# Performance work log

Hardware: AMD Instinct MI355X
Metric: run time of the kernel (lower is better)

## Reference

```python
import jax, jax.numpy as jnp
import numpy as np

N_NODES = 100000
N_EDGES = 1600000
IN_C, HID_C, OUT_C = 128, 128, 64


def setup_inputs() -> dict:
    key = jax.random.key(0)
    k1, k2, k3, k4 = jax.random.split(key, 4)
    x = jax.random.normal(k1, (N_NODES, IN_C), dtype=jnp.float32)
    edge_index = jax.random.randint(k2, (2, N_EDGES), 0, N_NODES, dtype=jnp.int32)
    # Glorot-style init scale for the linear weights (matches PyG GCNConv default)
    W1 = jax.random.normal(k3, (IN_C, HID_C), dtype=jnp.float32) * (1.0 / np.sqrt(IN_C))
    b1 = jnp.zeros((HID_C,), dtype=jnp.float32)
    W2 = jax.random.normal(k4, (HID_C, OUT_C), dtype=jnp.float32) * (1.0 / np.sqrt(HID_C))
    b2 = jnp.zeros((OUT_C,), dtype=jnp.float32)
    return {"x": x, "edge_index": edge_index, "W1": W1, "b1": b1, "W2": W2, "b2": b2}


def _gcn_norm(edge_index, num_nodes):
    """Add self-loops and compute symmetric normalization deg^-1/2[src]*deg^-1/2[dst]."""
    src, dst = edge_index[0], edge_index[1]
    loop = jnp.arange(num_nodes, dtype=src.dtype)
    src_f = jnp.concatenate([src, loop])
    dst_f = jnp.concatenate([dst, loop])
    ones = jnp.ones_like(dst_f, dtype=jnp.float32)
    deg = jax.ops.segment_sum(ones, dst_f, num_segments=num_nodes)  # in-degree incl. self-loop
    deg_inv_sqrt = jnp.where(deg > 0, jax.lax.rsqrt(deg), 0.0)
    norm = deg_inv_sqrt[src_f] * deg_inv_sqrt[dst_f]  # [E+N]
    return src_f, dst_f, norm


def _gcn_conv(x, W, b, src_f, dst_f, norm, num_nodes):
    h = x @ W                              # [N, C_out] linear transform first
    msg = h[src_f] * norm[:, None]         # gather + scale, [E+N, C_out]
    agg = jax.ops.segment_sum(msg, dst_f, num_segments=num_nodes)  # scatter-add
    return agg + b


def reference(x, edge_index, W1, b1, W2, b2):
    n = x.shape[0]
    src_f, dst_f, norm = _gcn_norm(edge_index, n)
    h = jax.nn.relu(_gcn_conv(x, W1, b1, src_f, dst_f, norm, n))
    out = _gcn_conv(h, W2, b2, src_f, dst_f, norm, n)
    return out
```

## Files before the change

kernel.cpp:

```cpp
#include <hip/hip_runtime.h>


constexpr int BLK = 256;
constexpr int PCAP = 2560;
constexpr int CPAD = 16;
constexpr int CHUNK = 6144;
constexpr int NBMAX = 800;


__global__ __launch_bounds__(256)
void bucket_sort_kernel(const int* __restrict__ src, const int* __restrict__ dst,
                        int* __restrict__ bcnt, unsigned* __restrict__ ebuf,
                        int e, int nbuck) {
    __shared__ unsigned stage[CHUNK];
    __shared__ unsigned short keys[CHUNK];
    __shared__ int hist[NBMAX];
    __shared__ int excl[NBMAX];
    __shared__ int gbase[NBMAX];
    __shared__ int wsum[256];

    const int t = threadIdx.x;
    const int base = blockIdx.x * CHUNK;
    const int cnt = min(CHUNK, e - base);

    for (int i = t; i < nbuck; i += 256) hist[i] = 0;
    __syncthreads();

    for (int i = t; i < cnt; i += 256) atomicAdd(&hist[dst[base + i] >> 7], 1);
    __syncthreads();

    const int b0 = t * 4;
    int s0 = 0, s1 = 0, s2 = 0, s3 = 0;
    if (b0 < nbuck)     s0 = hist[b0];
    if (b0 + 1 < nbuck) s1 = hist[b0 + 1];
    if (b0 + 2 < nbuck) s2 = hist[b0 + 2];
    if (b0 + 3 < nbuck) s3 = hist[b0 + 3];
    wsum[t] = s0 + s1 + s2 + s3;
    __syncthreads();
    for (int off = 1; off < 256; off <<= 1) {
        int v = (t >= off) ? wsum[t - off] : 0;
        __syncthreads();
        wsum[t] += v;
        __syncthreads();
    }
    int run = (t > 0) ? wsum[t - 1] : 0;
    if (b0 < nbuck)     { excl[b0]     = run; hist[b0]     = run; run += s0; }
    if (b0 + 1 < nbuck) { excl[b0 + 1] = run; hist[b0 + 1] = run; run += s1; }
    if (b0 + 2 < nbuck) { excl[b0 + 2] = run; hist[b0 + 2] = run; run += s2; }
    if (b0 + 3 < nbuck) { excl[b0 + 3] = run; hist[b0 + 3] = run; run += s3; }
    __syncthreads();

    for (int i = t; i < cnt; i += 256) {
        int s = src[base + i], d = dst[base + i];
        int bb = d >> 7;
        int p = atomicAdd(&hist[bb], 1);
        stage[p] = ((unsigned)s << 7) | (unsigned)(d & 127);
        keys[p] = (unsigned short)bb;
    }
    __syncthreads();

    if (b0 < nbuck)     { int c = hist[b0]     - excl[b0];     gbase[b0]     = c ? atomicAdd(&bcnt[b0 * CPAD], c)       : 0; }
    if (b0 + 1 < nbuck) { int c = hist[b0 + 1] - excl[b0 + 1]; gbase[b0 + 1] = c ? atomicAdd(&bcnt[(b0 + 1) * CPAD], c) : 0; }
    if (b0 + 2 < nbuck) { int c = hist[b0 + 2] - excl[b0 + 2]; gbase[b0 + 2] = c ? atomicAdd(&bcnt[(b0 + 2) * CPAD], c) : 0; }
    if (b0 + 3 < nbuck) { int c = hist[b0 + 3] - excl[b0 + 3]; gbase[b0 + 3] = c ? atomicAdd(&bcnt[(b0 + 3) * CPAD], c) : 0; }
    __syncthreads();

    for (int i = t; i < cnt; i += 256) {
        int bb = keys[i];
        int p = gbase[bb] + (i - excl[bb]);
        if (p < PCAP) ebuf[(size_t)bb * PCAP + p] = stage[i];
    }
}


__global__ __launch_bounds__(256)
void build_kernel(const unsigned* __restrict__ ebuf, const int* __restrict__ bcnt,
                  float* __restrict__ dis, int2* __restrict__ rp,
                  int* __restrict__ esrc, int n) {
    __shared__ int packed[PCAP];
    __shared__ int stage[PCAP];
    __shared__ int hist[128];
    __shared__ int excl[128];
    __shared__ int cur[128];

    const int b = blockIdx.x, t = threadIdx.x;
    const int base = b << 7;
    const int nloc = min(128, n - base);
    const int tot = min(bcnt[b * CPAD], PCAP);

    if (t < 128) hist[t] = 0;
    __syncthreads();

    const unsigned* eb = ebuf + (size_t)b * PCAP;
    for (int i = t; i < tot; i += 256) {
        int v = (int)eb[i];
        packed[i] = v;
        atomicAdd(&hist[v & 127], 1);
    }
    __syncthreads();

    if (t < 128) excl[t] = hist[t];
    __syncthreads();
    for (int off = 1; off < 128; off <<= 1) {
        int v = (t >= off && t < 128) ? excl[t - off] : 0;
        __syncthreads();
        if (t < 128) excl[t] += v;
        __syncthreads();
    }

    if (t < 128) {
        int deg = hist[t];
        int start = excl[t] - deg;
        cur[t] = start;
        if (t < nloc) {
            dis[base + t] = rsqrtf((float)(deg + 1));
            int gs = b * PCAP + start;
            rp[base + t] = make_int2(gs, gs + deg);
        }
    }
    __syncthreads();

    for (int i = t; i < tot; i += 256) {
        int v = packed[i];
        int p = atomicAdd(&cur[v & 127], 1);
        stage[p] = v >> 7;
    }
    __syncthreads();

    for (int i = t; i < tot; i += 256) esrc[b * PCAP + i] = stage[i];
}


__device__ __forceinline__ unsigned short f2bf(float f) {
    unsigned u = __float_as_uint(f);
    u += 0x7fffu + ((u >> 16) & 1u);
    return (unsigned short)(u >> 16);
}
__device__ __forceinline__ float bflo(unsigned u) { return __uint_as_float(u << 16); }
__device__ __forceinline__ float bfhi(unsigned u) { return __uint_as_float(u & 0xffff0000u); }
__device__ __forceinline__ unsigned pk2(short a, short b) {
    return (unsigned)(unsigned short)a | ((unsigned)(unsigned short)b << 16);
}

__device__ __forceinline__ void split2(float v, short& hi, short& lo) {
    unsigned short h = f2bf(v);
    float hf = __uint_as_float(((unsigned)h) << 16);
    hi = (short)h;
    lo = (short)f2bf(v - hf);
}

typedef __attribute__((ext_vector_type(8))) short bf16x8;
typedef __attribute__((ext_vector_type(4))) float f32x4;
#define MFMA_B16(a, b, c) __builtin_amdgcn_mfma_f32_16x16x32_bf16(a, b, c, 0, 0, 0)

__device__ __forceinline__ void split8(const float4& a, const float4& b, bf16x8& h, bf16x8& l) {
    short hh, ll;
    split2(a.x, hh, ll); h[0] = hh; l[0] = ll;
    split2(a.y, hh, ll); h[1] = hh; l[1] = ll;
    split2(a.z, hh, ll); h[2] = hh; l[2] = ll;
    split2(a.w, hh, ll); h[3] = hh; l[3] = ll;
    split2(b.x, hh, ll); h[4] = hh; l[4] = ll;
    split2(b.y, hh, ll); h[5] = hh; l[5] = ll;
    split2(b.z, hh, ll); h[6] = hh; l[6] = ll;
    split2(b.w, hh, ll); h[7] = hh; l[7] = ll;
}


__global__ void prep_b_kernel(const float* __restrict__ W1, const float* __restrict__ W2,
                              unsigned short* __restrict__ B1h, unsigned short* __restrict__ B1l,
                              unsigned short* __restrict__ B2h, unsigned short* __restrict__ B2l) {
    const int c = blockIdx.x;
    const int k = threadIdx.x;
    short h, l;
    if (c < 128) {
        split2(W1[(size_t)k * 128 + c], h, l);
        B1h[c * 128 + k] = (unsigned short)h;
        B1l[c * 128 + k] = (unsigned short)l;
    } else {
        const int c2 = c - 128;
        split2(W2[(size_t)k * 64 + c2], h, l);
        B2h[c2 * 128 + k] = (unsigned short)h;
        B2l[c2 * 128 + k] = (unsigned short)l;
    }
}


constexpr int BAS = 72;

template <int COLS, bool PRESPLIT>
__global__ __launch_bounds__(256, 4)
void gemm_mfma(const float* __restrict__ Af, const unsigned short* __restrict__ Ah,
               const unsigned short* __restrict__ Al,
               const unsigned short* __restrict__ Bh, const unsigned short* __restrict__ Bl,
               const float* __restrict__ dis, unsigned* __restrict__ Cb, int nrows) {
    constexpr int CT = COLS / 16;
    constexpr int BE = COLS * BAS;
    constexpr int CSC = COLS + 8;
    constexpr int SMEM = (2 * BE * 2 > 128 * CSC * 2) ? 2 * BE * 2 : 128 * CSC * 2;

    __shared__ __align__(16) char smem[SMEM];
    short* sBh = (short*)smem;
    short* sBl = sBh + BE;

    const int t = threadIdx.x;
    const int rowbase = blockIdx.x * 128;
    const int wave = t >> 6;
    const int lane = t & 63;
    const int quad = lane >> 4;
    const int l16 = lane & 15;

    const int gr0 = rowbase + wave * 32 + l16;
    const int gr1 = gr0 + 16;

    f32x4 acc[2][CT];
#pragma unroll
    for (int rt = 0; rt < 2; ++rt)
#pragma unroll
        for (int ct = 0; ct < CT; ++ct) {
            f32x4 z = {0.f, 0.f, 0.f, 0.f};
            acc[rt][ct] = z;
        }

    for (int half = 0; half < 2; ++half) {
        {
            constexpr int NV = COLS * 8;
            uint4* dh = (uint4*)sBh;
            uint4* dl = (uint4*)sBl;
            const uint4* gh = (const uint4*)Bh;
            const uint4* gl = (const uint4*)Bl;
            for (int idx = t; idx < NV; idx += 256) {
                int c = idx >> 3, kq = idx & 7;
                int gidx = c * 16 + half * 8 + kq;
                int didx = c * 9 + kq;
                dh[didx] = gh[gidx];
                dl[didx] = gl[gidx];
            }
        }
        __syncthreads();

#pragma unroll
        for (int kc = 0; kc < 2; ++kc) {
            const int ko = kc * 32 + quad * 8;
            bf16x8 ah0, al0, ah1, al1;
            if constexpr (PRESPLIT) {
                bf16x8 z = {0, 0, 0, 0, 0, 0, 0, 0};
                ah0 = z; al0 = z; ah1 = z; al1 = z;
                if (gr0 < nrows) {
                    ah0 = *(const bf16x8*)&Ah[(size_t)gr0 * 128 + half * 64 + ko];
                    al0 = *(const bf16x8*)&Al[(size_t)gr0 * 128 + half * 64 + ko];
                }
                if (gr1 < nrows) {
                    ah1 = *(const bf16x8*)&Ah[(size_t)gr1 * 128 + half * 64 + ko];
                    al1 = *(const bf16x8*)&Al[(size_t)gr1 * 128 + half * 64 + ko];
                }
            } else {
                float4 va = {0.f, 0.f, 0.f, 0.f}, vb = va, vc = va, vd = va;
                if (gr0 < nrows) {
                    const float4* ap = (const float4*)(Af + (size_t)gr0 * 128 + half * 64 + ko);
                    va = ap[0]; vb = ap[1];
                }
                if (gr1 < nrows) {
                    const float4* ap = (const float4*)(Af + (size_t)gr1 * 128 + half * 64 + ko);
                    vc = ap[0]; vd = ap[1];
                }
                split8(va, vb, ah0, al0);
                split8(vc, vd, ah1, al1);
            }
#pragma unroll
            for (int ct = 0; ct < CT; ++ct) {
                const int bo = (ct * 16 + l16) * BAS + ko;
                bf16x8 bh = *(const bf16x8*)&sBh[bo];
                bf16x8 bl = *(const bf16x8*)&sBl[bo];
                acc[0][ct] = MFMA_B16(ah0, bh, acc[0][ct]);
                acc[1][ct] = MFMA_B16(ah1, bh, acc[1][ct]);
                acc[0][ct] = MFMA_B16(al0, bh, acc[0][ct]);
                acc[1][ct] = MFMA_B16(al1, bh, acc[1][ct]);
                acc[0][ct] = MFMA_B16(ah0, bl, acc[0][ct]);
                acc[1][ct] = MFMA_B16(ah1, bl, acc[1][ct]);
            }
        }
        __syncthreads();
    }

    short* Cs = (short*)smem;
    float sv[2][4];
#pragma unroll
    for (int rt = 0; rt < 2; ++rt)
#pragma unroll
        for (int r = 0; r < 4; ++r) {
            int rr = rowbase + wave * 32 + rt * 16 + quad * 4 + r;
            sv[rt][r] = (rr < nrows) ? dis[rr] : 0.f;
        }
#pragma unroll
    for (int rt = 0; rt < 2; ++rt)
#pragma unroll
        for (int ct = 0; ct < CT; ++ct) {
            const int rb = wave * 32 + rt * 16 + quad * 4;
            const int c = ct * 16 + l16;
#pragma unroll
            for (int r = 0; r < 4; ++r)
                Cs[(rb + r) * CSC + c] = (short)f2bf(sv[rt][r] * acc[rt][ct][r]);
        }
    __syncthreads();

    {
        const int row = t >> 1, hf = t & 1;
        const int gr = rowbase + row;
        if (gr < nrows) {
            const uint4* cr = (const uint4*)&Cs[row * CSC + hf * (COLS / 2)];
            uint4* dstp = (uint4*)Cb + (size_t)gr * (COLS / 8) + hf * (COLS / 16);
#pragma unroll
            for (int i = 0; i < COLS / 16; ++i) dstp[i] = cr[i];
        }
    }
}


template <int C, bool SPLITOUT>
__global__ __launch_bounds__(256)
void gather_add_kernel(const int2* __restrict__ rp, const int* __restrict__ esrc,
                       const float* __restrict__ dis, const unsigned* __restrict__ hs,
                       const float* __restrict__ bias, float* __restrict__ out,
                       unsigned short* __restrict__ outh, unsigned short* __restrict__ outl,
                       int n) {
    constexpr int L = C / 8;
    const int gid = blockIdx.x * BLK + threadIdx.x;
    const int node = gid / L;
    const int lane = gid % L;
    if (node >= n) return;

    const uint4* h4 = (const uint4*)hs;
    const int2 se = rp[node];

    float acc[8];
    {
        uint4 v = h4[(size_t)node * L + lane];
        acc[0] = bflo(v.x); acc[1] = bfhi(v.x);
        acc[2] = bflo(v.y); acc[3] = bfhi(v.y);
        acc[4] = bflo(v.z); acc[5] = bfhi(v.z);
        acc[6] = bflo(v.w); acc[7] = bfhi(v.w);
    }

#define ACC8(v)                                           \
    acc[0] += bflo(v.x); acc[1] += bfhi(v.x);             \
    acc[2] += bflo(v.y); acc[3] += bfhi(v.y);             \
    acc[4] += bflo(v.z); acc[5] += bfhi(v.z);             \
    acc[6] += bflo(v.w); acc[7] += bfhi(v.w);

    int k = se.x;
    const int end = se.y;
    for (; k + 3 < end; k += 4) {
        int s0 = esrc[k], s1 = esrc[k + 1], s2 = esrc[k + 2], s3 = esrc[k + 3];
        uint4 v0 = h4[(size_t)s0 * L + lane];
        uint4 v1 = h4[(size_t)s1 * L + lane];
        uint4 v2 = h4[(size_t)s2 * L + lane];
        uint4 v3 = h4[(size_t)s3 * L + lane];
        ACC8(v0) ACC8(v1) ACC8(v2) ACC8(v3)
    }
    for (; k < end; ++k) {
        uint4 v = h4[(size_t)esrc[k] * L + lane];
        ACC8(v)
    }
#undef ACC8

    const float di = dis[node];
    const float4 bj0 = ((const float4*)bias)[lane * 2 + 0];
    const float4 bj1 = ((const float4*)bias)[lane * 2 + 1];
    float v0 = fmaf(di, acc[0], bj0.x), v1 = fmaf(di, acc[1], bj0.y);
    float v2 = fmaf(di, acc[2], bj0.z), v3 = fmaf(di, acc[3], bj0.w);
    float v4 = fmaf(di, acc[4], bj1.x), v5 = fmaf(di, acc[5], bj1.y);
    float v6 = fmaf(di, acc[6], bj1.z), v7 = fmaf(di, acc[7], bj1.w);

    if constexpr (SPLITOUT) {
        short h0, l0, h1, l1, h2, l2, h3, l3, h4s, l4, h5, l5, h6, l6, h7, l7;
        split2(fmaxf(v0, 0.f), h0, l0); split2(fmaxf(v1, 0.f), h1, l1);
        split2(fmaxf(v2, 0.f), h2, l2); split2(fmaxf(v3, 0.f), h3, l3);
        split2(fmaxf(v4, 0.f), h4s, l4); split2(fmaxf(v5, 0.f), h5, l5);
        split2(fmaxf(v6, 0.f), h6, l6); split2(fmaxf(v7, 0.f), h7, l7);
        uint4 oh, ol;
        oh.x = pk2(h0, h1); oh.y = pk2(h2, h3); oh.z = pk2(h4s, h5); oh.w = pk2(h6, h7);
        ol.x = pk2(l0, l1); ol.y = pk2(l2, l3); ol.z = pk2(l4, l5);  ol.w = pk2(l6, l7);
        ((uint4*)outh)[(size_t)node * L + lane] = oh;
        ((uint4*)outl)[(size_t)node * L + lane] = ol;
    } else {
        float4 o0 = make_float4(v0, v1, v2, v3);
        float4 o1 = make_float4(v4, v5, v6, v7);
        float4* o4 = (float4*)out;
        o4[(size_t)node * (C / 4) + lane * 2 + 0] = o0;
        o4[(size_t)node * (C / 4) + lane * 2 + 1] = o1;
    }
}


extern "C" void kernel_launch(void* const* d_in, const int* in_sizes, int n_in,
                              void* d_out, int out_size, void* d_ws, size_t ws_size,
                              hipStream_t stream) {
    const float* x  = (const float*)d_in[0];
    const int*   ei = (const int*)d_in[1];
    const float* W1 = (const float*)d_in[2];
    const float* b1 = (const float*)d_in[3];
    const float* W2 = (const float*)d_in[4];
    const float* b2 = (const float*)d_in[5];
    float* out = (float*)d_out;

    const int n = in_sizes[0] / 128;
    const int e = in_sizes[1] / 2;
    const int* src = ei;
    const int* dst = ei + e;

    char* ws = (char*)d_ws;
    float*    dis  = (float*)   (ws + 0x0);
    int2*     rp   = (int2*)    (ws + 0x80000);
    int*      bcnt = (int*)     (ws + 0x180000);
    unsigned short* B1h = (unsigned short*)(ws + 0x1A0000);
    unsigned short* B1l = (unsigned short*)(ws + 0x1A8000);
    unsigned short* B2h = (unsigned short*)(ws + 0x1B0000);
    unsigned short* B2l = (unsigned short*)(ws + 0x1B4000);
    int*      esrc = (int*)     (ws + 0x280000);
    unsigned* hb   = (unsigned*)(ws + 0xB00000);
    unsigned short* A2h = (unsigned short*)(ws + 0x2400000);
    unsigned short* A2l = (unsigned short*)(ws + 0x3C80000);
    unsigned* ebuf = (unsigned*)(ws + 0x2400000);
    unsigned* h2b  = hb;

    const int nbuck = (n + 127) >> 7;
    const int nb_g = (n + 127) / 128;

    hipMemsetAsync(bcnt, 0, (size_t)nbuck * CPAD * 4, stream);
    prep_b_kernel<<<192, 128, 0, stream>>>(W1, W2, B1h, B1l, B2h, B2l);
    bucket_sort_kernel<<<(e + CHUNK - 1) / CHUNK, 256, 0, stream>>>(src, dst, bcnt, ebuf, e, nbuck);
    build_kernel<<<nbuck, 256, 0, stream>>>(ebuf, bcnt, dis, rp, esrc, n);

    gemm_mfma<128, false><<<nb_g, 256, 0, stream>>>(x, nullptr, nullptr, B1h, B1l, dis, hb, n);
    gather_add_kernel<128, true><<<(n * 16 + BLK - 1) / BLK, BLK, 0, stream>>>(
        rp, esrc, dis, hb, b1, nullptr, A2h, A2l, n);

    gemm_mfma<64, true><<<nb_g, 256, 0, stream>>>(nullptr, A2h, A2l, B2h, B2l, dis, h2b, n);
    gather_add_kernel<64, false><<<(n * 8 + BLK - 1) / BLK, BLK, 0, stream>>>(
        rp, esrc, dis, h2b, b2, out, nullptr, nullptr, n);
}
```

Measured before the change: 274.5 us.

## Fuse layer-1 aggregation with layer-2 GEMM and widen per-thread gather work

Layer-1 neighbor aggregation is fused with the layer-2 MFMA GEMM. Each block aggregates 32 nodes, writes the ReLU'd hi/lo bf16 split into LDS, and multiplies by W2 directly. This removes the global write and re-read of the split A2 activations and one kernel launch. Both gather kernels now give each thread 16 channels instead of 8, so fewer threads share a node, which changes memory-level parallelism and register pressure. In the fused kernel the B2 fragments are read straight from global memory rather than staged in LDS.

Measured after the change: 266.4 us. 3.0% less time.

```diff
diff --git a/kernel.cpp b/kernel.cpp
--- a/kernel.cpp
+++ b/kernel.cpp
@@ -187,12 +187,11 @@
 
 constexpr int BAS = 72;
 
-template <int COLS, bool PRESPLIT>
 __global__ __launch_bounds__(256, 4)
-void gemm_mfma(const float* __restrict__ Af, const unsigned short* __restrict__ Ah,
-               const unsigned short* __restrict__ Al,
+void gemm_mfma(const float* __restrict__ Af,
                const unsigned short* __restrict__ Bh, const unsigned short* __restrict__ Bl,
                const float* __restrict__ dis, unsigned* __restrict__ Cb, int nrows) {
+    constexpr int COLS = 128;
     constexpr int CT = COLS / 16;
     constexpr int BE = COLS * BAS;
     constexpr int CSC = COLS + 8;
@@ -242,30 +241,17 @@
         for (int kc = 0; kc < 2; ++kc) {
             const int ko = kc * 32 + quad * 8;
             bf16x8 ah0, al0, ah1, al1;
-            if constexpr (PRESPLIT) {
-                bf16x8 z = {0, 0, 0, 0, 0, 0, 0, 0};
-                ah0 = z; al0 = z; ah1 = z; al1 = z;
-                if (gr0 < nrows) {
-                    ah0 = *(const bf16x8*)&Ah[(size_t)gr0 * 128 + half * 64 + ko];
-                    al0 = *(const bf16x8*)&Al[(size_t)gr0 * 128 + half * 64 + ko];
-                }
-                if (gr1 < nrows) {
-                    ah1 = *(const bf16x8*)&Ah[(size_t)gr1 * 128 + half * 64 + ko];
-                    al1 = *(const bf16x8*)&Al[(size_t)gr1 * 128 + half * 64 + ko];
-                }
-            } else {
-                float4 va = {0.f, 0.f, 0.f, 0.f}, vb = va, vc = va, vd = va;
-                if (gr0 < nrows) {
-                    const float4* ap = (const float4*)(Af + (size_t)gr0 * 128 + half * 64 + ko);
-                    va = ap[0]; vb = ap[1];
-                }
-                if (gr1 < nrows) {
-                    const float4* ap = (const float4*)(Af + (size_t)gr1 * 128 + half * 64 + ko);
-                    vc = ap[0]; vd = ap[1];
-                }
-                split8(va, vb, ah0, al0);
-                split8(vc, vd, ah1, al1);
-            }
+            float4 va = {0.f, 0.f, 0.f, 0.f}, vb = va, vc = va, vd = va;
+            if (gr0 < nrows) {
+                const float4* ap = (const float4*)(Af + (size_t)gr0 * 128 + half * 64 + ko);
+                va = ap[0]; vb = ap[1];
+            }
+            if (gr1 < nrows) {
+                const float4* ap = (const float4*)(Af + (size_t)gr1 * 128 + half * 64 + ko);
+                vc = ap[0]; vd = ap[1];
+            }
+            split8(va, vb, ah0, al0);
+            split8(vc, vd, ah1, al1);
 #pragma unroll
             for (int ct = 0; ct < CT; ++ct) {
                 const int bo = (ct * 16 + l16) * BAS + ko;
@@ -316,80 +302,220 @@
 }
 
 
-template <int C, bool SPLITOUT>
-__global__ __launch_bounds__(256)
-void gather_add_kernel(const int2* __restrict__ rp, const int* __restrict__ esrc,
-                       const float* __restrict__ dis, const unsigned* __restrict__ hs,
-                       const float* __restrict__ bias, float* __restrict__ out,
-                       unsigned short* __restrict__ outh, unsigned short* __restrict__ outl,
-                       int n) {
-    constexpr int L = C / 8;
-    const int gid = blockIdx.x * BLK + threadIdx.x;
-    const int node = gid / L;
-    const int lane = gid % L;
-    if (node >= n) return;
-
-    const uint4* h4 = (const uint4*)hs;
-    const int2 se = rp[node];
-
-    float acc[8];
-    {
-        uint4 v = h4[(size_t)node * L + lane];
-        acc[0] = bflo(v.x); acc[1] = bfhi(v.x);
-        acc[2] = bflo(v.y); acc[3] = bfhi(v.y);
-        acc[4] = bflo(v.z); acc[5] = bfhi(v.z);
-        acc[6] = bflo(v.w); acc[7] = bfhi(v.w);
-    }
-
-#define ACC8(v)                                           \
+#define ACCLO(v)                                          \
     acc[0] += bflo(v.x); acc[1] += bfhi(v.x);             \
     acc[2] += bflo(v.y); acc[3] += bfhi(v.y);             \
     acc[4] += bflo(v.z); acc[5] += bfhi(v.z);             \
     acc[6] += bflo(v.w); acc[7] += bfhi(v.w);
+#define ACCHI(v)                                          \
+    acc[8]  += bflo(v.x); acc[9]  += bfhi(v.x);           \
+    acc[10] += bflo(v.y); acc[11] += bfhi(v.y);           \
+    acc[12] += bflo(v.z); acc[13] += bfhi(v.z);           \
+    acc[14] += bflo(v.w); acc[15] += bfhi(v.w);
+
+__global__ __launch_bounds__(256)
+void gather_gemm_kernel(const int2* __restrict__ rp, const int* __restrict__ esrc,
+                        const float* __restrict__ dis, const unsigned* __restrict__ hs,
+                        const float* __restrict__ bias,
+                        const unsigned short* __restrict__ B2h,
+                        const unsigned short* __restrict__ B2l,
+                        unsigned* __restrict__ h2b, int n) {
+    constexpr int ASTR = 136;
+    constexpr int CSTR = 72;
+    __shared__ __align__(16) short sAh[32 * ASTR];
+    __shared__ __align__(16) short sAl[32 * ASTR];
+
+    const int t = threadIdx.x;
+    const int base = blockIdx.x * 32;
+
+    {
+        const int nl = t >> 3;
+        const int l8 = t & 7;
+        const int node = base + nl;
+        if (node < n) {
+            const uint4* h4 = (const uint4*)hs;
+            const int2 se = rp[node];
+            float acc[16];
+            {
+                uint4 v0 = h4[(size_t)node * 16 + l8];
+                uint4 v1 = h4[(size_t)node * 16 + 8 + l8];
+                acc[0] = bflo(v0.x); acc[1] = bfhi(v0.x);
+                acc[2] = bflo(v0.y); acc[3] = bfhi(v0.y);
+                acc[4] = bflo(v0.z); acc[5] = bfhi(v0.z);
+                acc[6] = bflo(v0.w); acc[7] = bfhi(v0.w);
+                acc[8]  = bflo(v1.x); acc[9]  = bfhi(v1.x);
+                acc[10] = bflo(v1.y); acc[11] = bfhi(v1.y);
+                acc[12] = bflo(v1.z); acc[13] = bfhi(v1.z);
+                acc[14] = bflo(v1.w); acc[15] = bfhi(v1.w);
+            }
+            int k = se.x;
+            const int end = se.y;
+            for (; k + 3 < end; k += 4) {
+                int s0 = esrc[k], s1 = esrc[k + 1], s2 = esrc[k + 2], s3 = esrc[k + 3];
+                uint4 a0 = h4[(size_t)s0 * 16 + l8], b0 = h4[(size_t)s0 * 16 + 8 + l8];
+                uint4 a1 = h4[(size_t)s1 * 16 + l8], b1 = h4[(size_t)s1 * 16 + 8 + l8];
+                uint4 a2 = h4[(size_t)s2 * 16 + l8], b2 = h4[(size_t)s2 * 16 + 8 + l8];
+                uint4 a3 = h4[(size_t)s3 * 16 + l8], b3 = h4[(size_t)s3 * 16 + 8 + l8];
+                ACCLO(a0) ACCHI(b0) ACCLO(a1) ACCHI(b1)
+                ACCLO(a2) ACCHI(b2) ACCLO(a3) ACCHI(b3)
+            }
+            for (; k < end; ++k) {
+                int s = esrc[k];
+                uint4 a = h4[(size_t)s * 16 + l8], b = h4[(size_t)s * 16 + 8 + l8];
+                ACCLO(a) ACCHI(b)
+            }
+
+            const float di = dis[node];
+            const float4* b4 = (const float4*)bias;
+            float4 ba = b4[l8 * 2], bb = b4[l8 * 2 + 1];
+            float4 bc = b4[16 + l8 * 2], bd = b4[17 + l8 * 2];
+            float v[16];
+            v[0]  = fmaxf(fmaf(di, acc[0],  ba.x), 0.f);
+            v[1]  = fmaxf(fmaf(di, acc[1],  ba.y), 0.f);
+            v[2]  = fmaxf(fmaf(di, acc[2],  ba.z), 0.f);
+            v[3]  = fmaxf(fmaf(di, acc[3],  ba.w), 0.f);
+            v[4]  = fmaxf(fmaf(di, acc[4],  bb.x), 0.f);
+            v[5]  = fmaxf(fmaf(di, acc[5],  bb.y), 0.f);
+            v[6]  = fmaxf(fmaf(di, acc[6],  bb.z), 0.f);
+            v[7]  = fmaxf(fmaf(di, acc[7],  bb.w), 0.f);
+            v[8]  = fmaxf(fmaf(di, acc[8],  bc.x), 0.f);
+            v[9]  = fmaxf(fmaf(di, acc[9],  bc.y), 0.f);
+            v[10] = fmaxf(fmaf(di, acc[10], bc.z), 0.f);
+            v[11] = fmaxf(fmaf(di, acc[11], bc.w), 0.f);
+            v[12] = fmaxf(fmaf(di, acc[12], bd.x), 0.f);
+            v[13] = fmaxf(fmaf(di, acc[13], bd.y), 0.f);
+            v[14] = fmaxf(fmaf(di, acc[14], bd.z), 0.f);
+            v[15] = fmaxf(fmaf(di, acc[15], bd.w), 0.f);
+
+            short h0, l0, h1, l1, h2, l2, h3, l3, h4v, l4, h5, l5, h6, l6, h7, l7;
+            uint4 oh, ol;
+            split2(v[0], h0, l0); split2(v[1], h1, l1); split2(v[2], h2, l2); split2(v[3], h3, l3);
+            split2(v[4], h4v, l4); split2(v[5], h5, l5); split2(v[6], h6, l6); split2(v[7], h7, l7);
+            oh.x = pk2(h0, h1); oh.y = pk2(h2, h3); oh.z = pk2(h4v, h5); oh.w = pk2(h6, h7);
+            ol.x = pk2(l0, l1); ol.y = pk2(l2, l3); ol.z = pk2(l4, l5);  ol.w = pk2(l6, l7);
+            *(uint4*)&sAh[nl * ASTR + l8 * 8] = oh;
+            *(uint4*)&sAl[nl * ASTR + l8 * 8] = ol;
+            split2(v[8], h0, l0); split2(v[9], h1, l1); split2(v[10], h2, l2); split2(v[11], h3, l3);
+            split2(v[12], h4v, l4); split2(v[13], h5, l5); split2(v[14], h6, l6); split2(v[15], h7, l7);
+            oh.x = pk2(h0, h1); oh.y = pk2(h2, h3); oh.z = pk2(h4v, h5); oh.w = pk2(h6, h7);
+            ol.x = pk2(l0, l1); ol.y = pk2(l2, l3); ol.z = pk2(l4, l5);  ol.w = pk2(l6, l7);
+            *(uint4*)&sAh[nl * ASTR + 64 + l8 * 8] = oh;
+            *(uint4*)&sAl[nl * ASTR + 64 + l8 * 8] = ol;
+        } else {
+            uint4 z = {0u, 0u, 0u, 0u};
+            *(uint4*)&sAh[nl * ASTR + l8 * 8] = z;
+            *(uint4*)&sAl[nl * ASTR + l8 * 8] = z;
+            *(uint4*)&sAh[nl * ASTR + 64 + l8 * 8] = z;
+            *(uint4*)&sAl[nl * ASTR + 64 + l8 * 8] = z;
+        }
+    }
+    __syncthreads();
+
+    const int wave = t >> 6, lane = t & 63, quad = lane >> 4, l16 = lane & 15;
+    const int col = wave * 16 + l16;
+    f32x4 c0 = {0.f, 0.f, 0.f, 0.f}, c1 = c0;
+#pragma unroll
+    for (int ks = 0; ks < 4; ++ks) {
+        const int ko = ks * 32 + quad * 8;
+        bf16x8 bh = *(const bf16x8*)&B2h[col * 128 + ko];
+        bf16x8 bl = *(const bf16x8*)&B2l[col * 128 + ko];
+        bf16x8 ah0 = *(const bf16x8*)&sAh[l16 * ASTR + ko];
+        bf16x8 al0 = *(const bf16x8*)&sAl[l16 * ASTR + ko];
+        bf16x8 ah1 = *(const bf16x8*)&sAh[(16 + l16) * ASTR + ko];
+        bf16x8 al1 = *(const bf16x8*)&sAl[(16 + l16) * ASTR + ko];
+        c0 = MFMA_B16(ah0, bh, c0);
+        c1 = MFMA_B16(ah1, bh, c1);
+        c0 = MFMA_B16(al0, bh, c0);
+        c1 = MFMA_B16(al1, bh, c1);
+        c0 = MFMA_B16(ah0, bl, c0);
+        c1 = MFMA_B16(ah1, bl, c1);
+    }
+    __syncthreads();
+
+    short* Cs = sAh;
+#pragma unroll
+    for (int r = 0; r < 4; ++r) {
+        const int row0 = quad * 4 + r, row1 = 16 + quad * 4 + r;
+        const float d0 = (base + row0 < n) ? dis[base + row0] : 0.f;
+        const float d1 = (base + row1 < n) ? dis[base + row1] : 0.f;
+        Cs[row0 * CSTR + col] = (short)f2bf(d0 * c0[r]);
+        Cs[row1 * CSTR + col] = (short)f2bf(d1 * c1[r]);
+    }
+    __syncthreads();
+    {
+        const int row = t >> 3, l8 = t & 7;
+        const int gr = base + row;
+        if (gr < n)
+            ((uint4*)h2b)[(size_t)gr * 8 + l8] = *(const uint4*)&Cs[row * CSTR + l8 * 8];
+    }
+}
+
+
+__global__ __launch_bounds__(256)
+void gather_out_kernel(const int2* __restrict__ rp, const int* __restrict__ esrc,
+                       const float* __restrict__ dis, const unsigned* __restrict__ hs,
+                       const float* __restrict__ bias, float* __restrict__ out, int n) {
+    const int gid = blockIdx.x * BLK + threadIdx.x;
+    const int node = gid >> 2;
+    const int l4 = gid & 3;
+    if (node >= n) return;
+
+    const uint4* h4 = (const uint4*)hs;
+    const int2 se = rp[node];
+
+    float acc[16];
+    {
+        uint4 v0 = h4[(size_t)node * 8 + l4];
+        uint4 v1 = h4[(size_t)node * 8 + 4 + l4];
+        acc[0] = bflo(v0.x); acc[1] = bfhi(v0.x);
+        acc[2] = bflo(v0.y); acc[3] = bfhi(v0.y);
+        acc[4] = bflo(v0.z); acc[5] = bfhi(v0.z);
+        acc[6] = bflo(v0.w); acc[7] = bfhi(v0.w);
+        acc[8]  = bflo(v1.x); acc[9]  = bfhi(v1.x);
+        acc[10] = bflo(v1.y); acc[11] = bfhi(v1.y);
+        acc[12] = bflo(v1.z); acc[13] = bfhi(v1.z);
+        acc[14] = bflo(v1.w); acc[15] = bfhi(v1.w);
+    }
 
     int k = se.x;
     const int end = se.y;
     for (; k + 3 < end; k += 4) {
         int s0 = esrc[k], s1 = esrc[k + 1], s2 = esrc[k + 2], s3 = esrc[k + 3];
-        uint4 v0 = h4[(size_t)s0 * L + lane];
-        uint4 v1 = h4[(size_t)s1 * L + lane];
-        uint4 v2 = h4[(size_t)s2 * L + lane];
-        uint4 v3 = h4[(size_t)s3 * L + lane];
-        ACC8(v0) ACC8(v1) ACC8(v2) ACC8(v3)
+        uint4 a0 = h4[(size_t)s0 * 8 + l4], b0 = h4[(size_t)s0 * 8 + 4 + l4];
+        uint4 a1 = h4[(size_t)s1 * 8 + l4], b1 = h4[(size_t)s1 * 8 + 4 + l4];
+        uint4 a2 = h4[(size_t)s2 * 8 + l4], b2 = h4[(size_t)s2 * 8 + 4 + l4];
+        uint4 a3 = h4[(size_t)s3 * 8 + l4], b3 = h4[(size_t)s3 * 8 + 4 + l4];
+        ACCLO(a0) ACCHI(b0) ACCLO(a1) ACCHI(b1)
+        ACCLO(a2) ACCHI(b2) ACCLO(a3) ACCHI(b3)
     }
     for (; k < end; ++k) {
-        uint4 v = h4[(size_t)esrc[k] * L + lane];
-        ACC8(v)
-    }
-#undef ACC8
+        int s = esrc[k];
+        uint4 a = h4[(size_t)s * 8 + l4], b = h4[(size_t)s * 8 + 4 + l4];
+        ACCLO(a) ACCHI(b)
+    }
 
     const float di = dis[node];
-    const float4 bj0 = ((const float4*)bias)[lane * 2 + 0];
-    const float4 bj1 = ((const float4*)bias)[lane * 2 + 1];
-    float v0 = fmaf(di, acc[0], bj0.x), v1 = fmaf(di, acc[1], bj0.y);
-    float v2 = fmaf(di, acc[2], bj0.z), v3 = fmaf(di, acc[3], bj0.w);
-    float v4 = fmaf(di, acc[4], bj1.x), v5 = fmaf(di, acc[5], bj1.y);
-    float v6 = fmaf(di, acc[6], bj1.z), v7 = fmaf(di, acc[7], bj1.w);
-
-    if constexpr (SPLITOUT) {
-        short h0, l0, h1, l1, h2, l2, h3, l3, h4s, l4, h5, l5, h6, l6, h7, l7;
-        split2(fmaxf(v0, 0.f), h0, l0); split2(fmaxf(v1, 0.f), h1, l1);
-        split2(fmaxf(v2, 0.f), h2, l2); split2(fmaxf(v3, 0.f), h3, l3);
-        split2(fmaxf(v4, 0.f), h4s, l4); split2(fmaxf(v5, 0.f), h5, l5);
-        split2(fmaxf(v6, 0.f), h6, l6); split2(fmaxf(v7, 0.f), h7, l7);
-        uint4 oh, ol;
-        oh.x = pk2(h0, h1); oh.y = pk2(h2, h3); oh.z = pk2(h4s, h5); oh.w = pk2(h6, h7);
-        ol.x = pk2(l0, l1); ol.y = pk2(l2, l3); ol.z = pk2(l4, l5);  ol.w = pk2(l6, l7);
-        ((uint4*)outh)[(size_t)node * L + lane] = oh;
-        ((uint4*)outl)[(size_t)node * L + lane] = ol;
-    } else {
-        float4 o0 = make_float4(v0, v1, v2, v3);
-        float4 o1 = make_float4(v4, v5, v6, v7);
-        float4* o4 = (float4*)out;
-        o4[(size_t)node * (C / 4) + lane * 2 + 0] = o0;
-        o4[(size_t)node * (C / 4) + lane * 2 + 1] = o1;
-    }
-}
+    const float4* b4 = (const float4*)bias;
+    const float4 ba = b4[l4 * 2], bb = b4[l4 * 2 + 1];
+    const float4 bc = b4[8 + l4 * 2], bd = b4[9 + l4 * 2];
+    float4 o0, o1, o2, o3;
+    o0.x = fmaf(di, acc[0],  ba.x); o0.y = fmaf(di, acc[1],  ba.y);
+    o0.z = fmaf(di, acc[2],  ba.z); o0.w = fmaf(di, acc[3],  ba.w);
+    o1.x = fmaf(di, acc[4],  bb.x); o1.y = fmaf(di, acc[5],  bb.y);
+    o1.z = fmaf(di, acc[6],  bb.z); o1.w = fmaf(di, acc[7],  bb.w);
+    o2.x = fmaf(di, acc[8],  bc.x); o2.y = fmaf(di, acc[9],  bc.y);
+    o2.z = fmaf(di, acc[10], bc.z); o2.w = fmaf(di, acc[11], bc.w);
+    o3.x = fmaf(di, acc[12], bd.x); o3.y = fmaf(di, acc[13], bd.y);
+    o3.z = fmaf(di, acc[14], bd.z); o3.w = fmaf(di, acc[15], bd.w);
+    float4* o4 = (float4*)out;
+    o4[(size_t)node * 16 + l4 * 2]     = o0;
+    o4[(size_t)node * 16 + l4 * 2 + 1] = o1;
+    o4[(size_t)node * 16 + 8 + l4 * 2]     = o2;
+    o4[(size_t)node * 16 + 8 + l4 * 2 + 1] = o3;
+}
+
+#undef ACCLO
+#undef ACCHI
 
 
 extern "C" void kernel_launch(void* const* d_in, const int* in_sizes, int n_in,
@@ -418,10 +544,8 @@
     unsigned short* B2l = (unsigned short*)(ws + 0x1B4000);
     int*      esrc = (int*)     (ws + 0x280000);
     unsigned* hb   = (unsigned*)(ws + 0xB00000);
-    unsigned short* A2h = (unsigned short*)(ws + 0x2400000);
-    unsigned short* A2l = (unsigned short*)(ws + 0x3C80000);
+    unsigned* h2b  = (unsigned*)(ws + 0x2400000);
     unsigned* ebuf = (unsigned*)(ws + 0x2400000);
-    unsigned* h2b  = hb;
 
     const int nbuck = (n + 127) >> 7;
     const int nb_g = (n + 127) / 128;
@@ -431,11 +555,11 @@
     bucket_sort_kernel<<<(e + CHUNK - 1) / CHUNK, 256, 0, stream>>>(src, dst, bcnt, ebuf, e, nbuck);
     build_kernel<<<nbuck, 256, 0, stream>>>(ebuf, bcnt, dis, rp, esrc, n);
 
-    gemm_mfma<128, false><<<nb_g, 256, 0, stream>>>(x, nullptr, nullptr, B1h, B1l, dis, hb, n);
-    gather_add_kernel<128, true><<<(n * 16 + BLK - 1) / BLK, BLK, 0, stream>>>(
-        rp, esrc, dis, hb, b1, nullptr, A2h, A2l, n);
-
-    gemm_mfma<64, true><<<nb_g, 256, 0, stream>>>(nullptr, A2h, A2l, B2h, B2l, dis, h2b, n);
-    gather_add_kernel<64, false><<<(n * 8 + BLK - 1) / BLK, BLK, 0, stream>>>(
-        rp, esrc, dis, h2b, b2, out, nullptr, nullptr, n);
-}
+    gemm_mfma<<<nb_g, 256, 0, stream>>>(x, B1h, B1l, dis, hb, n);
+
+    gather_gemm_kernel<<<(n + 31) / 32, 256, 0, stream>>>(
+        rp, esrc, dis, hb, b1, B2h, B2l, h2b, n);
+
+    gather_out_kernel<<<(n * 4 + BLK - 1) / BLK, BLK, 0, stream>>>(
+        rp, esrc, dis, h2b, b2, out, n);
+}
```
